# Kernel tuning notes

Measured on AMD Instinct MI355X. Metric: run time of the kernel, lower is better.

Reference implementation:

```python
import jax, jax.numpy as jnp
import numpy as np

D_MODEL = 1024
N_HEADS = 16
D_K = D_MODEL // N_HEADS
MIN_F = 3
MAX_F = 10


def setup_inputs() -> dict:
    key = jax.random.key(0)
    ks = jax.random.split(key, 9)
    B, L = 4, 8192
    x = jax.random.normal(ks[0], (B, L, D_MODEL), jnp.float32)
    def w(k):
        return jax.random.normal(k, (D_MODEL, D_MODEL), jnp.float32) * 0.02
    def b(k):
        return jax.random.normal(k, (D_MODEL,), jnp.float32) * 0.02
    return {
        'x': x,
        'wq': w(ks[1]), 'bq': b(ks[2]),
        'wk': w(ks[3]), 'bk': b(ks[4]),
        'wv': w(ks[5]), 'bv': b(ks[6]),
        'wo': w(ks[7]), 'bo': b(ks[8]),
    }


def _sparsity_score(Q):
    # Q: (B, H, L, d_k)
    l2 = jnp.linalg.norm(Q, axis=-1)
    logp = jax.nn.log_softmax(Q, axis=-1)
    prob = jnp.exp(logp)
    entropy = -jnp.sum(prob * jnp.log(prob + 1e-9), axis=-1)
    var = jnp.var(Q, axis=-1, ddof=1)  # torch.var is unbiased by default
    return 0.5 * l2 + 0.3 * entropy + 0.2 * var


def reference(x, wq, bq, wk, bk, wv, bv, wo, bo):
    B, L, D = x.shape
    H, dk = N_HEADS, D_K
    # torch Linear: y = x @ W.T + b
    Q = (x @ wq.T + bq).reshape(B, L, H, dk).transpose(0, 2, 1, 3)  # (B,H,L,dk)
    K = (x @ wk.T + bk).reshape(B, L, H, dk).transpose(0, 2, 1, 3)
    V = (x @ wv.T + bv).reshape(B, L, H, dk).transpose(0, 2, 1, 3)

    q_scores = _sparsity_score(Q)  # (B,H,L)
    q_std = jnp.std(q_scores, axis=2, keepdims=True, ddof=1)
    q_mean = jnp.mean(q_scores, axis=2, keepdims=True)
    factor = jnp.clip(
        jnp.round(q_std / (q_mean + 1e-6) * MAX_F).astype(jnp.int32),
        MIN_F, MAX_F)  # (B,H,1)
    u = factor[:, 0, 0]  # per-batch k, taken from head 0 (matches torch code)

    # Fixed-size top-k of MAX_F; rows beyond u are masked to zero.
    _, top_idx = jax.lax.top_k(q_scores, MAX_F)  # (B,H,MAX_F)
    mask = (jnp.arange(MAX_F)[None, None, :] < u[:, None, None])  # (B,1->H,MAX_F)

    Q_sparse = jnp.take_along_axis(Q, top_idx[..., None], axis=2)  # (B,H,MAX_F,dk)
    scores = jnp.einsum('bhud,bhld->bhul', Q_sparse, K) / np.sqrt(dk).astype(np.float32)
    attn = jax.nn.softmax(scores, axis=-1)
    out = jnp.einsum('bhul,bhld->bhud', attn, V)  # (B,H,MAX_F,dk)
    out = out * mask[..., None].astype(out.dtype)

    # Scatter back into zeros; top-k indices are distinct per (b,h), so writing
    # masked zeros at the extra indices leaves those rows zero as in torch.
    bi = jnp.arange(B)[:, None, None]
    hi = jnp.arange(H)[None, :, None]
    full = jnp.zeros((B, H, L, dk), out.dtype).at[bi, hi, top_idx].set(out)

    merged = full.transpose(0, 2, 1, 3).reshape(B, L, D)
    return merged @ wo.T + bo
```

## Files before the change

### kernel.cpp

```cpp
#include <hip/hip_runtime.h>
#include <cmath>


typedef short     s16x8 __attribute__((ext_vector_type(8)));
typedef unsigned short u16x8 __attribute__((ext_vector_type(8)));
typedef unsigned short u16x4 __attribute__((ext_vector_type(4)));
typedef float     f32x4 __attribute__((ext_vector_type(4)));

__device__ __forceinline__ unsigned short f2bf(float f) {
    unsigned u = __float_as_uint(f);
    u += 0x7fffu + ((u >> 16) & 1u);
    return (unsigned short)(u >> 16);
}
__device__ __forceinline__ float bf2f(unsigned short s) {
    return __uint_as_float(((unsigned)s) << 16);
}

__device__ __forceinline__ void async16(const void* g, void* l) {
    __builtin_amdgcn_global_load_lds(
        (const __attribute__((address_space(1))) void*)g,
        (__attribute__((address_space(3))) void*)l, 16, 0, 0);
}

__global__ void k_conv(const float* __restrict__ x, const float* __restrict__ wq,
                       const float* __restrict__ wk, const float* __restrict__ wv,
                       unsigned short* __restrict__ xb, unsigned short* __restrict__ wb) {
    size_t i = (size_t)blockIdx.x * 256 + threadIdx.x;
    if (i < 8388608) {
        float4 v = ((const float4*)x)[i];
        ushort4 o; o.x = f2bf(v.x); o.y = f2bf(v.y); o.z = f2bf(v.z); o.w = f2bf(v.w);
        ((ushort4*)xb)[i] = o;
    } else {
        size_t j = i - 8388608;
        size_t wsel = j >> 18, rem = j & 262143;
        const float* src = wsel == 0 ? wq : (wsel == 1 ? wk : wv);
        float4 v = ((const float4*)src)[rem];
        ushort4 o; o.x = f2bf(v.x); o.y = f2bf(v.y); o.z = f2bf(v.z); o.w = f2bf(v.w);
        ((ushort4*)wb)[j] = o;
    }
}

__global__ __launch_bounds__(256) void k_gemm_qkv(
    const unsigned short* __restrict__ xb, const unsigned short* __restrict__ wb,
    const float* __restrict__ bq, const float* __restrict__ bk, const float* __restrict__ bv,
    unsigned short* __restrict__ Kb, unsigned short* __restrict__ Vb,
    float* __restrict__ scores)
{
    __shared__ unsigned short As[128 * 32];
    __shared__ unsigned short Bs[128 * 32];
    int bid = blockIdx.x;
    int mt = bid / 24, rem = bid % 24;
    int wsel = rem >> 3, nt = rem & 7;
    const unsigned short* wbase = wb + ((size_t)wsel << 20) + ((size_t)nt * 128) * 1024;
    const float* bias = wsel == 0 ? bq : (wsel == 1 ? bk : bv);
    unsigned short* outp = wsel == 1 ? Kb : Vb;
    int tid = threadIdx.x, wave = tid >> 6, lane = tid & 63;
    int ml = lane & 15, quad = lane >> 4, wm = wave >> 1, wn = wave & 1;
    int lr = lane >> 2, lc = lane & 3;
    const unsigned short* xbase = xb + ((size_t)mt * 128) * 1024;

    f32x4 acc[4][4] = {};
    for (int k0 = 0; k0 < 1024; k0 += 32) {
#pragma unroll
        for (int s = 0; s < 2; ++s) {
            int seg = wave * 2 + s;
            int row = seg * 16 + lr;
            async16(xbase + (size_t)row * 1024 + k0 + lc * 8, &As[seg * 512]);
            async16(wbase + (size_t)row * 1024 + k0 + lc * 8, &Bs[seg * 512]);
        }
        __builtin_amdgcn_s_waitcnt(0);
        __syncthreads();
        s16x8 a[4], b[4];
#pragma unroll
        for (int i = 0; i < 4; ++i) a[i] = *(const s16x8*)&As[(wm * 64 + i * 16 + ml) * 32 + quad * 8];
#pragma unroll
        for (int j = 0; j < 4; ++j) b[j] = *(const s16x8*)&Bs[(wn * 64 + j * 16 + ml) * 32 + quad * 8];
#pragma unroll
        for (int i = 0; i < 4; ++i)
#pragma unroll
            for (int j = 0; j < 4; ++j)
                acc[i][j] = __builtin_amdgcn_mfma_f32_16x16x32_bf16(a[i], b[j], acc[i][j], 0, 0, 0);
        __syncthreads();
    }

    float bvv[4];
#pragma unroll
    for (int j = 0; j < 4; ++j) bvv[j] = bias[nt * 128 + wn * 64 + j * 16 + ml];

    if (wsel == 0) {
        int hh = nt * 2 + wn;
#pragma unroll
        for (int i = 0; i < 4; ++i) {
#pragma unroll
            for (int r = 0; r < 4; ++r) {
                float q0 = acc[i][0][r] + bvv[0];
                float q1 = acc[i][1][r] + bvv[1];
                float q2 = acc[i][2][r] + bvv[2];
                float q3 = acc[i][3][r] + bvv[3];
                float mx = fmaxf(fmaxf(q0, q1), fmaxf(q2, q3));
                float sm = q0 + q1 + q2 + q3;
                float ss = q0 * q0 + q1 * q1 + q2 * q2 + q3 * q3;
#pragma unroll
                for (int off = 1; off < 16; off <<= 1) {
                    mx = fmaxf(mx, __shfl_xor(mx, off));
                    sm += __shfl_xor(sm, off);
                    ss += __shfl_xor(ss, off);
                }
                float e0 = expf(q0 - mx), e1 = expf(q1 - mx);
                float e2 = expf(q2 - mx), e3 = expf(q3 - mx);
                float S = e0 + e1 + e2 + e3;
#pragma unroll
                for (int off = 1; off < 16; off <<= 1) S += __shfl_xor(S, off);
                float is = 1.f / S;
                float p0 = e0 * is, p1 = e1 * is, p2 = e2 * is, p3 = e3 * is;
                float ent = -p0 * logf(p0 + 1e-9f) - p1 * logf(p1 + 1e-9f)
                            - p2 * logf(p2 + 1e-9f) - p3 * logf(p3 + 1e-9f);
                float mean = sm * (1.f / 64.f);
                float d0 = q0 - mean, d1 = q1 - mean, d2 = q2 - mean, d3 = q3 - mean;
                float var = d0 * d0 + d1 * d1 + d2 * d2 + d3 * d3;
#pragma unroll
                for (int off = 1; off < 16; off <<= 1) {
                    ent += __shfl_xor(ent, off);
                    var += __shfl_xor(var, off);
                }
                if (ml == 0) {
                    float sc = 0.5f * sqrtf(ss) + 0.3f * ent + 0.2f * (var * (1.f / 63.f));
                    int row = mt * 128 + wm * 64 + i * 16 + quad * 4 + r;
                    scores[(size_t)(((row >> 13) << 4) + hh) * 8192 + (row & 8191)] = sc;
                }
            }
        }
    } else {
#pragma unroll
        for (int i = 0; i < 4; ++i) {
            int grow0 = mt * 128 + wm * 64 + i * 16 + quad * 4;
#pragma unroll
            for (int j = 0; j < 4; ++j) {
                int gcol = nt * 128 + wn * 64 + j * 16 + ml;
#pragma unroll
                for (int r = 0; r < 4; ++r)
                    outp[(size_t)(grow0 + r) * 1024 + gcol] = f2bf(acc[i][j][r] + bvv[j]);
            }
        }
    }
}

__global__ __launch_bounds__(1024) void k_cand(const float* __restrict__ scores,
                                               int* __restrict__ cand, int* __restrict__ u)
{
    int pair = blockIdx.x; int t = threadIdx.x;
    __shared__ float  s_lds[8192];
    __shared__ double dred[1024];
    __shared__ float  wvv[16];
    __shared__ int    wii[16];
    const float* sp = scores + (size_t)pair * 8192;
    for (int i = t; i < 8192; i += 1024) s_lds[i] = sp[i];
    __syncthreads();

    if ((pair & 15) == 0) {
        double a0 = 0;
#pragma unroll
        for (int k = 0; k < 8; ++k) a0 += (double)s_lds[t + k * 1024];
        dred[t] = a0; __syncthreads();
        for (int st = 512; st > 0; st >>= 1) { if (t < st) dred[t] += dred[t + st]; __syncthreads(); }
        double mean = dred[0] / 8192.0;
        __syncthreads();
        double a1 = 0;
#pragma unroll
        for (int k = 0; k < 8; ++k) { double d = (double)s_lds[t + k * 1024] - mean; a1 += d * d; }
        dred[t] = a1; __syncthreads();
        for (int st = 512; st > 0; st >>= 1) { if (t < st) dred[t] += dred[t + st]; __syncthreads(); }
        if (t == 0) {
            double sd = sqrt(dred[0] / 8191.0);
            double ratio = sd / (mean + 1e-6) * 10.0;
            int f = (int)rint(ratio);
            f = f < 3 ? 3 : (f > 10 ? 10 : f);
            u[pair >> 4] = f;
        }
        __syncthreads();
    }

    for (int it = 0; it < 16; ++it) {
        float bv = -1e30f; int bi = 0x7fffffff;
#pragma unroll
        for (int k = 0; k < 8; ++k) {
            int i = t + k * 1024;
            float v = s_lds[i];
            if (v > bv || (v == bv && i < bi)) { bv = v; bi = i; }
        }
#pragma unroll
        for (int off = 32; off > 0; off >>= 1) {
            float ov = __shfl_down(bv, off);
            int   oi = __shfl_down(bi, off);
            if (ov > bv || (ov == bv && oi < bi)) { bv = ov; bi = oi; }
        }
        if ((t & 63) == 0) { wvv[t >> 6] = bv; wii[t >> 6] = bi; }
        __syncthreads();
        if (t == 0) {
            float fv = wvv[0]; int fi = wii[0];
            for (int k = 1; k < 16; ++k)
                if (wvv[k] > fv || (wvv[k] == fv && wii[k] < fi)) { fv = wvv[k]; fi = wii[k]; }
            cand[pair * 16 + it] = fi;
            s_lds[fi] = -1e30f;
        }
        __syncthreads();
    }
}

__global__ __launch_bounds__(256) void k_rescore(
    const int* __restrict__ cand, const float* __restrict__ x,
    const float* __restrict__ wq, const float* __restrict__ bq,
    double* __restrict__ cscore, float* __restrict__ cq)
{
    int bid = blockIdx.x;
    int pair = bid >> 4;
    int b = pair >> 4, h = pair & 15;
    int t = threadIdx.x;
    __shared__ float  xrow[1024];
    __shared__ double dred[256];
    __shared__ double qrow[64];

    int l = cand[bid];
    const float* xr = x + ((size_t)b * 8192 + l) * 1024;
    for (int i = t; i < 1024; i += 256) xrow[i] = xr[i];
    __syncthreads();

    int d = t >> 2, ks = t & 3;
    const float* wr = wq + (size_t)(h * 64 + d) * 1024 + ks * 256;
    const float* xs = xrow + ks * 256;
    double p = 0;
    for (int k = 0; k < 256; k += 4) {
        float4 w4 = *(const float4*)(wr + k);
        float4 x4 = *(const float4*)(xs + k);
        p += (double)w4.x * x4.x + (double)w4.y * x4.y +
             (double)w4.z * x4.z + (double)w4.w * x4.w;
    }
    dred[t] = p; __syncthreads();
    if ((t & 3) == 0)
        qrow[t >> 2] = dred[t] + dred[t + 1] + dred[t + 2] + dred[t + 3] + (double)bq[h * 64 + (t >> 2)];
    __syncthreads();

    if (t < 64) {
        double q = qrow[t];
        cq[(size_t)bid * 64 + t] = (float)q;
        double m = q;
#pragma unroll
        for (int off = 32; off > 0; off >>= 1) m = fmax(m, __shfl_down(m, off));
        m = __shfl(m, 0);
        double e = exp(q - m);
        double sum = q, sumsq = q * q, S = e;
#pragma unroll
        for (int off = 32; off > 0; off >>= 1) {
            sum += __shfl_down(sum, off);
            sumsq += __shfl_down(sumsq, off);
            S += __shfl_down(S, off);
        }
        sum = __shfl(sum, 0); sumsq = __shfl(sumsq, 0); S = __shfl(S, 0);
        double pp = e / S;
        double entc = -pp * log(pp + 1e-9);
        double mean = sum / 64.0;
        double dv = q - mean;
        double varc = dv * dv;
#pragma unroll
        for (int off = 32; off > 0; off >>= 1) {
            entc += __shfl_down(entc, off);
            varc += __shfl_down(varc, off);
        }
        if (t == 0)
            cscore[bid] = 0.5 * sqrt(sumsq) + 0.3 * entc + 0.2 * (varc / 63.0);
    }
}

__global__ void k_select(const int* __restrict__ cand, const double* __restrict__ cscore,
                         const float* __restrict__ cq,
                         int* __restrict__ sel, float* __restrict__ selq)
{
    int pair = blockIdx.x; int t = threadIdx.x;
    __shared__ int order[10];
    if (t == 0) {
        bool used[16] = {};
        for (int r = 0; r < 10; ++r) {
            int best = -1;
            for (int c = 0; c < 16; ++c) {
                if (used[c]) continue;
                int ic = pair * 16 + c;
                if (best < 0 || cscore[ic] > cscore[pair * 16 + best] ||
                    (cscore[ic] == cscore[pair * 16 + best] && cand[ic] < cand[pair * 16 + best]))
                    best = c;
            }
            used[best] = true; order[r] = best;
            sel[pair * 10 + r] = cand[pair * 16 + best];
        }
    }
    __syncthreads();
    for (int r = 0; r < 10; ++r)
        selq[((size_t)pair * 10 + r) * 64 + t] = cq[((size_t)pair * 16 + order[r]) * 64 + t];
}

__global__ __launch_bounds__(256) void k_attn_part(
    const unsigned short* __restrict__ Kb, const unsigned short* __restrict__ Vb,
    const float* __restrict__ selq, const int* __restrict__ u,
    float* __restrict__ part)
{
    int bid = blockIdx.x;
    int pair = bid >> 5, chunk = bid & 31;
    int b = pair >> 4, h = pair & 15;
    int uu = u[b];
    int t = threadIdx.x, wave = t >> 6, lane = t & 63;

    __shared__ float q_sh[10][64];
    __shared__ float w_sh[10][256];
    __shared__ unsigned short V_sh[256][68];
    __shared__ float mc_sh[10][2], Sc_sh[10][2];

    size_t kvbase = ((size_t)b * 8192 + (size_t)chunk * 256) * 1024 + h * 64;

    for (int i = t; i < uu * 64; i += 256)
        q_sh[i >> 6][i & 63] = selq[(size_t)pair * 640 + i] * 0.125f;

    const u16x8* kr = (const u16x8*)(Kb + kvbase + (size_t)t * 1024);
    const u16x8* vr = (const u16x8*)(Vb + kvbase + (size_t)t * 1024);
    u16x8 vreg[8];
#pragma unroll
    for (int k8 = 0; k8 < 8; ++k8) vreg[k8] = vr[k8];
#pragma unroll
    for (int k8 = 0; k8 < 8; ++k8) {
        *(u16x4*)&V_sh[t][k8 * 8]     = { vreg[k8][0], vreg[k8][1], vreg[k8][2], vreg[k8][3] };
        *(u16x4*)&V_sh[t][k8 * 8 + 4] = { vreg[k8][4], vreg[k8][5], vreg[k8][6], vreg[k8][7] };
    }
    float krow[64];
#pragma unroll
    for (int k8 = 0; k8 < 8; ++k8) {
        u16x8 kv = kr[k8];
#pragma unroll
        for (int e = 0; e < 8; ++e) krow[k8 * 8 + e] = bf2f(kv[e]);
    }
    __syncthreads();

    for (int rr = 0; rr < uu; ++rr) {
        const float4* qp = (const float4*)q_sh[rr];
        float acc = 0.f;
#pragma unroll
        for (int i4 = 0; i4 < 16; ++i4) {
            float4 q4 = qp[i4];
            acc += q4.x * krow[i4 * 4] + q4.y * krow[i4 * 4 + 1] +
                   q4.z * krow[i4 * 4 + 2] + q4.w * krow[i4 * 4 + 3];
        }
        w_sh[rr][t] = acc;
    }
    __syncthreads();

    for (int rr = wave; rr < uu; rr += 4) {
        float4 wv = *(const float4*)&w_sh[rr][lane * 4];
        float m4 = fmaxf(fmaxf(wv.x, wv.y), fmaxf(wv.z, wv.w));
#pragma unroll
        for (int off = 16; off > 0; off >>= 1) m4 = fmaxf(m4, __shfl_xor(m4, off));
        float e0 = expf(wv.x - m4), e1 = expf(wv.y - m4);
        float e2 = expf(wv.z - m4), e3 = expf(wv.w - m4);
        float s = e0 + e1 + e2 + e3;
#pragma unroll
        for (int off = 16; off > 0; off >>= 1) s += __shfl_xor(s, off);
        float4 ev = { e0, e1, e2, e3 };
        *(float4*)&w_sh[rr][lane * 4] = ev;
        if ((lane & 31) == 0) { int jh = lane >> 5; mc_sh[rr][jh] = m4; Sc_sh[rr][jh] = s; }
    }
    __syncthreads();

    int jh = t >> 7, tt = t & 127, dp = tt & 31;
    for (int rr = tt >> 5; rr < uu; rr += 4) {
        float o0 = 0.f, o1 = 0.f;
        int j0 = jh * 128;
        for (int j = j0; j < j0 + 128; j += 4) {
            float4 w4 = *(const float4*)&w_sh[rr][j];
#pragma unroll
            for (int jj = 0; jj < 4; ++jj) {
                unsigned v = *(const unsigned*)&V_sh[j + jj][dp * 2];
                float w1 = jj == 0 ? w4.x : (jj == 1 ? w4.y : (jj == 2 ? w4.z : w4.w));
                o0 += w1 * __uint_as_float(v << 16);
                o1 += w1 * __uint_as_float(v & 0xffff0000u);
            }
        }
        float* pp = part + (((size_t)pair * 10 + rr) * 64 + chunk * 2 + jh) * 66;
        float2 o2 = { o0, o1 };
        *(float2*)&pp[2 + dp * 2] = o2;
        if (dp == 0) { pp[0] = mc_sh[rr][jh]; pp[1] = Sc_sh[rr][jh]; }
    }
}

__global__ void k_bias(const float* __restrict__ bo, float* __restrict__ out) {
    size_t i = (size_t)blockIdx.x * 256 + threadIdx.x;
    int col4 = (int)(i & 255);
    ((float4*)out)[i] = ((const float4*)bo)[col4];
}

__global__ __launch_bounds__(256) void k_mergescatter(
    const float* __restrict__ part, const int* __restrict__ sel,
    const int* __restrict__ u, const float* __restrict__ wo,
    float* __restrict__ out)
{
    int idx = blockIdx.x; int pair = idx / 10; int r = idx % 10;
    int b = pair >> 4, h = pair & 15;
    if (r >= u[b]) return;
    int t = threadIdx.x;
    __shared__ float a_sh[64];
    if (t < 64) {
        const float* base = part + ((size_t)pair * 10 + r) * 64 * 66;
        float m = -1e30f;
        for (int c = 0; c < 64; ++c) m = fmaxf(m, base[c * 66]);
        float S = 0, o = 0;
        for (int c = 0; c < 64; ++c) {
            float f = expf(base[c * 66] - m);
            S += f * base[c * 66 + 1];
            o += f * base[c * 66 + 2 + t];
        }
        a_sh[t] = o / S;
    }
    __syncthreads();
    int l = sel[pair * 10 + r];
    float* orow = out + ((size_t)b * 8192 + l) * 1024;
    for (int j = t; j < 1024; j += 256) {
        const float* wr = wo + (size_t)j * 1024 + h * 64;
        float acc = 0;
#pragma unroll
        for (int d = 0; d < 64; d += 4) {
            float4 w4 = *(const float4*)(wr + d);
            acc += a_sh[d] * w4.x + a_sh[d + 1] * w4.y + a_sh[d + 2] * w4.z + a_sh[d + 3] * w4.w;
        }
        atomicAdd(orow + j, acc);
    }
}

static constexpr size_t OFF_XB    = 0;
static constexpr size_t OFF_WB    = OFF_XB + 67108864;
static constexpr size_t OFF_KB    = OFF_WB + 6291456;
static constexpr size_t OFF_VB    = OFF_KB + 67108864;
static constexpr size_t OFF_SC    = OFF_VB + 67108864;
static constexpr size_t OFF_U     = OFF_SC + 2097152;
static constexpr size_t OFF_SEL   = OFF_U + 256;
static constexpr size_t OFF_SELQ  = OFF_SEL + 4096;
static constexpr size_t OFF_PART  = OFF_SELQ + 163840;
static constexpr size_t OFF_CAND  = OFF_PART + 10813440;
static constexpr size_t OFF_CSC   = OFF_CAND + 4096;
static constexpr size_t OFF_CQ    = OFF_CSC + 8192;
static constexpr size_t WS_NEED   = OFF_CQ + 262144;

extern "C" void kernel_launch(void* const* d_in, const int* in_sizes, int n_in,
                              void* d_out, int out_size, void* d_ws, size_t ws_size,
                              hipStream_t stream)
{
    const float* x  = (const float*)d_in[0];
    const float* wq = (const float*)d_in[1];
    const float* bq = (const float*)d_in[2];
    const float* wk = (const float*)d_in[3];
    const float* bk = (const float*)d_in[4];
    const float* wv = (const float*)d_in[5];
    const float* bv = (const float*)d_in[6];
    const float* wo = (const float*)d_in[7];
    const float* bo = (const float*)d_in[8];
    float* out = (float*)d_out;

    if (ws_size < WS_NEED) return;

    char* ws = (char*)d_ws;
    unsigned short* xb = (unsigned short*)(ws + OFF_XB);
    unsigned short* wb = (unsigned short*)(ws + OFF_WB);
    unsigned short* Kb = (unsigned short*)(ws + OFF_KB);
    unsigned short* Vb = (unsigned short*)(ws + OFF_VB);
    float*  scores = (float*)(ws + OFF_SC);
    int*    u      = (int*)(ws + OFF_U);
    int*    sel    = (int*)(ws + OFF_SEL);
    float*  selq   = (float*)(ws + OFF_SELQ);
    float*  part   = (float*)(ws + OFF_PART);
    int*    cand   = (int*)(ws + OFF_CAND);
    double* cscore = (double*)(ws + OFF_CSC);
    float*  cq     = (float*)(ws + OFF_CQ);

    k_conv        <<<35840, 256,  0, stream>>>(x, wq, wk, wv, xb, wb);
    k_gemm_qkv    <<<6144,  256,  0, stream>>>(xb, wb, bq, bk, bv, Kb, Vb, scores);
    k_cand        <<<64,    1024, 0, stream>>>(scores, cand, u);
    k_rescore     <<<1024,  256,  0, stream>>>(cand, x, wq, bq, cscore, cq);
    k_select      <<<64,    64,   0, stream>>>(cand, cscore, cq, sel, selq);
    k_attn_part   <<<2048,  256,  0, stream>>>(Kb, Vb, selq, u, part);
    k_bias        <<<32768, 256,  0, stream>>>(bo, out);
    k_mergescatter<<<640,   256,  0, stream>>>(part, sel, u, wo, out);
}
```

Measured before the change: 733.8 us.

## Fuse candidate selection, rescoring and bias init kernels; simplify entropy math

```diff
diff --git a/kernel.cpp b/kernel.cpp
--- a/kernel.cpp
+++ b/kernel.cpp
@@ -22,21 +22,26 @@
         (__attribute__((address_space(3))) void*)l, 16, 0, 0);
 }
 
-__global__ void k_conv(const float* __restrict__ x, const float* __restrict__ wq,
-                       const float* __restrict__ wk, const float* __restrict__ wv,
-                       unsigned short* __restrict__ xb, unsigned short* __restrict__ wb) {
+__global__ void k_convbias(const float* __restrict__ x, const float* __restrict__ wq,
+                           const float* __restrict__ wk, const float* __restrict__ wv,
+                           const float* __restrict__ bo,
+                           unsigned short* __restrict__ xb, unsigned short* __restrict__ wb,
+                           float* __restrict__ out) {
     size_t i = (size_t)blockIdx.x * 256 + threadIdx.x;
     if (i < 8388608) {
         float4 v = ((const float4*)x)[i];
         ushort4 o; o.x = f2bf(v.x); o.y = f2bf(v.y); o.z = f2bf(v.z); o.w = f2bf(v.w);
         ((ushort4*)xb)[i] = o;
-    } else {
+    } else if (i < 9175040) {
         size_t j = i - 8388608;
         size_t wsel = j >> 18, rem = j & 262143;
         const float* src = wsel == 0 ? wq : (wsel == 1 ? wk : wv);
         float4 v = ((const float4*)src)[rem];
         ushort4 o; o.x = f2bf(v.x); o.y = f2bf(v.y); o.z = f2bf(v.z); o.w = f2bf(v.w);
         ((ushort4*)wb)[j] = o;
+    } else {
+        size_t j = i - 9175040;
+        ((float4*)out)[j] = ((const float4*)bo)[j & 255];
     }
 }
 
@@ -106,23 +111,21 @@
                     sm += __shfl_xor(sm, off);
                     ss += __shfl_xor(ss, off);
                 }
-                float e0 = expf(q0 - mx), e1 = expf(q1 - mx);
-                float e2 = expf(q2 - mx), e3 = expf(q3 - mx);
-                float S = e0 + e1 + e2 + e3;
-#pragma unroll
-                for (int off = 1; off < 16; off <<= 1) S += __shfl_xor(S, off);
-                float is = 1.f / S;
-                float p0 = e0 * is, p1 = e1 * is, p2 = e2 * is, p3 = e3 * is;
-                float ent = -p0 * logf(p0 + 1e-9f) - p1 * logf(p1 + 1e-9f)
-                            - p2 * logf(p2 + 1e-9f) - p3 * logf(p3 + 1e-9f);
+                float e0 = __expf(q0 - mx), e1 = __expf(q1 - mx);
+                float e2 = __expf(q2 - mx), e3 = __expf(q3 - mx);
+                float S  = e0 + e1 + e2 + e3;
+                float wsum = e0 * (q0 - mx) + e1 * (q1 - mx) + e2 * (q2 - mx) + e3 * (q3 - mx);
+#pragma unroll
+                for (int off = 1; off < 16; off <<= 1) {
+                    S    += __shfl_xor(S, off);
+                    wsum += __shfl_xor(wsum, off);
+                }
+                float ent = __logf(S) - wsum / S;
                 float mean = sm * (1.f / 64.f);
                 float d0 = q0 - mean, d1 = q1 - mean, d2 = q2 - mean, d3 = q3 - mean;
                 float var = d0 * d0 + d1 * d1 + d2 * d2 + d3 * d3;
 #pragma unroll
-                for (int off = 1; off < 16; off <<= 1) {
-                    ent += __shfl_xor(ent, off);
-                    var += __shfl_xor(var, off);
-                }
+                for (int off = 1; off < 16; off <<= 1) var += __shfl_xor(var, off);
                 if (ml == 0) {
                     float sc = 0.5f * sqrtf(ss) + 0.3f * ent + 0.2f * (var * (1.f / 63.f));
                     int row = mt * 128 + wm * 64 + i * 16 + quad * 4 + r;
@@ -145,14 +148,22 @@
     }
 }
 
-__global__ __launch_bounds__(1024) void k_cand(const float* __restrict__ scores,
-                                               int* __restrict__ cand, int* __restrict__ u)
+__global__ __launch_bounds__(1024) void k_candsel(
+    const float* __restrict__ scores, const float* __restrict__ x,
+    const float* __restrict__ wq, const float* __restrict__ bq,
+    int* __restrict__ u, int* __restrict__ sel, float* __restrict__ selq)
 {
-    int pair = blockIdx.x; int t = threadIdx.x;
+    int pair = blockIdx.x; int b = pair >> 4, h = pair & 15;
+    int t = threadIdx.x;
     __shared__ float  s_lds[8192];
     __shared__ double dred[1024];
     __shared__ float  wvv[16];
     __shared__ int    wii[16];
+    __shared__ int    cand_s[16];
+    __shared__ double dq[16][64];
+    __shared__ double csc[16];
+    __shared__ int    order[10];
+
     const float* sp = scores + (size_t)pair * 8192;
     for (int i = t; i < 8192; i += 1024) s_lds[i] = sp[i];
     __syncthreads();
@@ -200,101 +211,67 @@
             float fv = wvv[0]; int fi = wii[0];
             for (int k = 1; k < 16; ++k)
                 if (wvv[k] > fv || (wvv[k] == fv && wii[k] < fi)) { fv = wvv[k]; fi = wii[k]; }
-            cand[pair * 16 + it] = fi;
+            cand_s[it] = fi;
             s_lds[fi] = -1e30f;
         }
         __syncthreads();
     }
-}
-
-__global__ __launch_bounds__(256) void k_rescore(
-    const int* __restrict__ cand, const float* __restrict__ x,
-    const float* __restrict__ wq, const float* __restrict__ bq,
-    double* __restrict__ cscore, float* __restrict__ cq)
-{
-    int bid = blockIdx.x;
-    int pair = bid >> 4;
-    int b = pair >> 4, h = pair & 15;
-    int t = threadIdx.x;
-    __shared__ float  xrow[1024];
-    __shared__ double dred[256];
-    __shared__ double qrow[64];
-
-    int l = cand[bid];
+
+    int c = t >> 6, d = t & 63;
+    int l = cand_s[c];
     const float* xr = x + ((size_t)b * 8192 + l) * 1024;
-    for (int i = t; i < 1024; i += 256) xrow[i] = xr[i];
-    __syncthreads();
-
-    int d = t >> 2, ks = t & 3;
-    const float* wr = wq + (size_t)(h * 64 + d) * 1024 + ks * 256;
-    const float* xs = xrow + ks * 256;
-    double p = 0;
-    for (int k = 0; k < 256; k += 4) {
+    const float* wr = wq + (size_t)(h * 64 + d) * 1024;
+    double p0 = 0, p1 = 0, p2 = 0, p3 = 0;
+    for (int k = 0; k < 1024; k += 4) {
         float4 w4 = *(const float4*)(wr + k);
-        float4 x4 = *(const float4*)(xs + k);
-        p += (double)w4.x * x4.x + (double)w4.y * x4.y +
-             (double)w4.z * x4.z + (double)w4.w * x4.w;
-    }
-    dred[t] = p; __syncthreads();
-    if ((t & 3) == 0)
-        qrow[t >> 2] = dred[t] + dred[t + 1] + dred[t + 2] + dred[t + 3] + (double)bq[h * 64 + (t >> 2)];
-    __syncthreads();
-
-    if (t < 64) {
-        double q = qrow[t];
-        cq[(size_t)bid * 64 + t] = (float)q;
-        double m = q;
-#pragma unroll
-        for (int off = 32; off > 0; off >>= 1) m = fmax(m, __shfl_down(m, off));
-        m = __shfl(m, 0);
-        double e = exp(q - m);
-        double sum = q, sumsq = q * q, S = e;
-#pragma unroll
-        for (int off = 32; off > 0; off >>= 1) {
-            sum += __shfl_down(sum, off);
-            sumsq += __shfl_down(sumsq, off);
-            S += __shfl_down(S, off);
-        }
-        sum = __shfl(sum, 0); sumsq = __shfl(sumsq, 0); S = __shfl(S, 0);
-        double pp = e / S;
-        double entc = -pp * log(pp + 1e-9);
-        double mean = sum / 64.0;
-        double dv = q - mean;
-        double varc = dv * dv;
-#pragma unroll
-        for (int off = 32; off > 0; off >>= 1) {
-            entc += __shfl_down(entc, off);
-            varc += __shfl_down(varc, off);
-        }
-        if (t == 0)
-            cscore[bid] = 0.5 * sqrt(sumsq) + 0.3 * entc + 0.2 * (varc / 63.0);
-    }
-}
-
-__global__ void k_select(const int* __restrict__ cand, const double* __restrict__ cscore,
-                         const float* __restrict__ cq,
-                         int* __restrict__ sel, float* __restrict__ selq)
-{
-    int pair = blockIdx.x; int t = threadIdx.x;
-    __shared__ int order[10];
+        float4 x4 = *(const float4*)(xr + k);
+        p0 += (double)w4.x * x4.x; p1 += (double)w4.y * x4.y;
+        p2 += (double)w4.z * x4.z; p3 += (double)w4.w * x4.w;
+    }
+    double q = p0 + p1 + p2 + p3 + (double)bq[h * 64 + d];
+    dq[c][d] = q;
+    double m = q;
+#pragma unroll
+    for (int off = 32; off > 0; off >>= 1) m = fmax(m, __shfl_down(m, off));
+    m = __shfl(m, 0);
+    double e = exp(q - m);
+    double sum = q, sumsq = q * q, S = e;
+#pragma unroll
+    for (int off = 32; off > 0; off >>= 1) {
+        sum += __shfl_down(sum, off);
+        sumsq += __shfl_down(sumsq, off);
+        S += __shfl_down(S, off);
+    }
+    sum = __shfl(sum, 0); sumsq = __shfl(sumsq, 0); S = __shfl(S, 0);
+    double pp = e / S;
+    double entc = -pp * log(pp + 1e-9);
+    double mean = sum / 64.0;
+    double dv = q - mean;
+    double varc = dv * dv;
+#pragma unroll
+    for (int off = 32; off > 0; off >>= 1) {
+        entc += __shfl_down(entc, off);
+        varc += __shfl_down(varc, off);
+    }
+    if (d == 0) csc[c] = 0.5 * sqrt(sumsq) + 0.3 * entc + 0.2 * (varc / 63.0);
+    __syncthreads();
+
     if (t == 0) {
         bool used[16] = {};
         for (int r = 0; r < 10; ++r) {
             int best = -1;
-            for (int c = 0; c < 16; ++c) {
-                if (used[c]) continue;
-                int ic = pair * 16 + c;
-                if (best < 0 || cscore[ic] > cscore[pair * 16 + best] ||
-                    (cscore[ic] == cscore[pair * 16 + best] && cand[ic] < cand[pair * 16 + best]))
-                    best = c;
+            for (int cc = 0; cc < 16; ++cc) {
+                if (used[cc]) continue;
+                if (best < 0 || csc[cc] > csc[best] ||
+                    (csc[cc] == csc[best] && cand_s[cc] < cand_s[best])) best = cc;
             }
             used[best] = true; order[r] = best;
-            sel[pair * 10 + r] = cand[pair * 16 + best];
-        }
-    }
-    __syncthreads();
-    for (int r = 0; r < 10; ++r)
-        selq[((size_t)pair * 10 + r) * 64 + t] = cq[((size_t)pair * 16 + order[r]) * 64 + t];
+            sel[pair * 10 + r] = cand_s[best];
+        }
+    }
+    __syncthreads();
+    if (t < 640)
+        selq[(size_t)pair * 640 + t] = (float)dq[order[t >> 6]][t & 63];
 }
 
 __global__ __launch_bounds__(256) void k_attn_part(
@@ -355,8 +332,8 @@
         float m4 = fmaxf(fmaxf(wv.x, wv.y), fmaxf(wv.z, wv.w));
 #pragma unroll
         for (int off = 16; off > 0; off >>= 1) m4 = fmaxf(m4, __shfl_xor(m4, off));
-        float e0 = expf(wv.x - m4), e1 = expf(wv.y - m4);
-        float e2 = expf(wv.z - m4), e3 = expf(wv.w - m4);
+        float e0 = __expf(wv.x - m4), e1 = __expf(wv.y - m4);
+        float e2 = __expf(wv.z - m4), e3 = __expf(wv.w - m4);
         float s = e0 + e1 + e2 + e3;
 #pragma unroll
         for (int off = 16; off > 0; off >>= 1) s += __shfl_xor(s, off);
@@ -385,12 +362,6 @@
         *(float2*)&pp[2 + dp * 2] = o2;
         if (dp == 0) { pp[0] = mc_sh[rr][jh]; pp[1] = Sc_sh[rr][jh]; }
     }
-}
-
-__global__ void k_bias(const float* __restrict__ bo, float* __restrict__ out) {
-    size_t i = (size_t)blockIdx.x * 256 + threadIdx.x;
-    int col4 = (int)(i & 255);
-    ((float4*)out)[i] = ((const float4*)bo)[col4];
 }
 
 __global__ __launch_bounds__(256) void k_mergescatter(
@@ -409,7 +380,7 @@
         for (int c = 0; c < 64; ++c) m = fmaxf(m, base[c * 66]);
         float S = 0, o = 0;
         for (int c = 0; c < 64; ++c) {
-            float f = expf(base[c * 66] - m);
+            float f = __expf(base[c * 66] - m);
             S += f * base[c * 66 + 1];
             o += f * base[c * 66 + 2 + t];
         }
@@ -439,10 +410,7 @@
 static constexpr size_t OFF_SEL   = OFF_U + 256;
 static constexpr size_t OFF_SELQ  = OFF_SEL + 4096;
 static constexpr size_t OFF_PART  = OFF_SELQ + 163840;
-static constexpr size_t OFF_CAND  = OFF_PART + 10813440;
-static constexpr size_t OFF_CSC   = OFF_CAND + 4096;
-static constexpr size_t OFF_CQ    = OFF_CSC + 8192;
-static constexpr size_t WS_NEED   = OFF_CQ + 262144;
+static constexpr size_t WS_NEED   = OFF_PART + 10813440;
 
 extern "C" void kernel_launch(void* const* d_in, const int* in_sizes, int n_in,
                               void* d_out, int out_size, void* d_ws, size_t ws_size,
@@ -471,16 +439,10 @@
     int*    sel    = (int*)(ws + OFF_SEL);
     float*  selq   = (float*)(ws + OFF_SELQ);
     float*  part   = (float*)(ws + OFF_PART);
-    int*    cand   = (int*)(ws + OFF_CAND);
-    double* cscore = (double*)(ws + OFF_CSC);
-    float*  cq     = (float*)(ws + OFF_CQ);
-
-    k_conv        <<<35840, 256,  0, stream>>>(x, wq, wk, wv, xb, wb);
+
+    k_convbias    <<<68608, 256,  0, stream>>>(x, wq, wk, wv, bo, xb, wb, out);
     k_gemm_qkv    <<<6144,  256,  0, stream>>>(xb, wb, bq, bk, bv, Kb, Vb, scores);
-    k_cand        <<<64,    1024, 0, stream>>>(scores, cand, u);
-    k_rescore     <<<1024,  256,  0, stream>>>(cand, x, wq, bq, cscore, cq);
-    k_select      <<<64,    64,   0, stream>>>(cand, cscore, cq, sel, selq);
+    k_candsel     <<<64,    1024, 0, stream>>>(scores, x, wq, bq, u, sel, selq);
     k_attn_part   <<<2048,  256,  0, stream>>>(Kb, Vb, selq, u, part);
-    k_bias        <<<32768, 256,  0, stream>>>(bo, out);
     k_mergescatter<<<640,   256,  0, stream>>>(part, sel, u, wo, out);
 }
```

After: 839.0 us. 14.3% more time.

## Split sparsity scoring out of QKV GEMM and fuse bias fill into conversion

Applied to the files above, without the earlier changes.

```diff
diff --git a/kernel.cpp b/kernel.cpp
--- a/kernel.cpp
+++ b/kernel.cpp
@@ -22,29 +22,33 @@
         (__attribute__((address_space(3))) void*)l, 16, 0, 0);
 }
 
-__global__ void k_conv(const float* __restrict__ x, const float* __restrict__ wq,
-                       const float* __restrict__ wk, const float* __restrict__ wv,
-                       unsigned short* __restrict__ xb, unsigned short* __restrict__ wb) {
+__global__ void k_convbias(const float* __restrict__ x, const float* __restrict__ wq,
+                           const float* __restrict__ wk, const float* __restrict__ wv,
+                           const float* __restrict__ bo,
+                           unsigned short* __restrict__ xb, unsigned short* __restrict__ wb,
+                           float* __restrict__ out) {
     size_t i = (size_t)blockIdx.x * 256 + threadIdx.x;
     if (i < 8388608) {
         float4 v = ((const float4*)x)[i];
         ushort4 o; o.x = f2bf(v.x); o.y = f2bf(v.y); o.z = f2bf(v.z); o.w = f2bf(v.w);
         ((ushort4*)xb)[i] = o;
-    } else {
+    } else if (i < 9175040) {
         size_t j = i - 8388608;
         size_t wsel = j >> 18, rem = j & 262143;
         const float* src = wsel == 0 ? wq : (wsel == 1 ? wk : wv);
         float4 v = ((const float4*)src)[rem];
         ushort4 o; o.x = f2bf(v.x); o.y = f2bf(v.y); o.z = f2bf(v.z); o.w = f2bf(v.w);
         ((ushort4*)wb)[j] = o;
+    } else {
+        size_t j = i - 9175040;
+        ((float4*)out)[j] = ((const float4*)bo)[j & 255];
     }
 }
 
 __global__ __launch_bounds__(256) void k_gemm_qkv(
     const unsigned short* __restrict__ xb, const unsigned short* __restrict__ wb,
     const float* __restrict__ bq, const float* __restrict__ bk, const float* __restrict__ bv,
-    unsigned short* __restrict__ Kb, unsigned short* __restrict__ Vb,
-    float* __restrict__ scores)
+    unsigned short* __restrict__ Qb, unsigned short* __restrict__ Kb, unsigned short* __restrict__ Vb)
 {
     __shared__ unsigned short As[128 * 32];
     __shared__ unsigned short Bs[128 * 32];
@@ -53,7 +57,7 @@
     int wsel = rem >> 3, nt = rem & 7;
     const unsigned short* wbase = wb + ((size_t)wsel << 20) + ((size_t)nt * 128) * 1024;
     const float* bias = wsel == 0 ? bq : (wsel == 1 ? bk : bv);
-    unsigned short* outp = wsel == 1 ? Kb : Vb;
+    unsigned short* outp = wsel == 0 ? Qb : (wsel == 1 ? Kb : Vb);
     int tid = threadIdx.x, wave = tid >> 6, lane = tid & 63;
     int ml = lane & 15, quad = lane >> 4, wm = wave >> 1, wn = wave & 1;
     int lr = lane >> 2, lc = lane & 3;
@@ -82,66 +86,61 @@
                 acc[i][j] = __builtin_amdgcn_mfma_f32_16x16x32_bf16(a[i], b[j], acc[i][j], 0, 0, 0);
         __syncthreads();
     }
-
-    float bvv[4];
-#pragma unroll
-    for (int j = 0; j < 4; ++j) bvv[j] = bias[nt * 128 + wn * 64 + j * 16 + ml];
-
-    if (wsel == 0) {
-        int hh = nt * 2 + wn;
-#pragma unroll
-        for (int i = 0; i < 4; ++i) {
-#pragma unroll
-            for (int r = 0; r < 4; ++r) {
-                float q0 = acc[i][0][r] + bvv[0];
-                float q1 = acc[i][1][r] + bvv[1];
-                float q2 = acc[i][2][r] + bvv[2];
-                float q3 = acc[i][3][r] + bvv[3];
-                float mx = fmaxf(fmaxf(q0, q1), fmaxf(q2, q3));
-                float sm = q0 + q1 + q2 + q3;
-                float ss = q0 * q0 + q1 * q1 + q2 * q2 + q3 * q3;
-#pragma unroll
-                for (int off = 1; off < 16; off <<= 1) {
-                    mx = fmaxf(mx, __shfl_xor(mx, off));
-                    sm += __shfl_xor(sm, off);
-                    ss += __shfl_xor(ss, off);
-                }
-                float e0 = expf(q0 - mx), e1 = expf(q1 - mx);
-                float e2 = expf(q2 - mx), e3 = expf(q3 - mx);
-                float S = e0 + e1 + e2 + e3;
-#pragma unroll
-                for (int off = 1; off < 16; off <<= 1) S += __shfl_xor(S, off);
-                float is = 1.f / S;
-                float p0 = e0 * is, p1 = e1 * is, p2 = e2 * is, p3 = e3 * is;
-                float ent = -p0 * logf(p0 + 1e-9f) - p1 * logf(p1 + 1e-9f)
-                            - p2 * logf(p2 + 1e-9f) - p3 * logf(p3 + 1e-9f);
-                float mean = sm * (1.f / 64.f);
-                float d0 = q0 - mean, d1 = q1 - mean, d2 = q2 - mean, d3 = q3 - mean;
-                float var = d0 * d0 + d1 * d1 + d2 * d2 + d3 * d3;
-#pragma unroll
-                for (int off = 1; off < 16; off <<= 1) {
-                    ent += __shfl_xor(ent, off);
-                    var += __shfl_xor(var, off);
-                }
-                if (ml == 0) {
-                    float sc = 0.5f * sqrtf(ss) + 0.3f * ent + 0.2f * (var * (1.f / 63.f));
-                    int row = mt * 128 + wm * 64 + i * 16 + quad * 4 + r;
-                    scores[(size_t)(((row >> 13) << 4) + hh) * 8192 + (row & 8191)] = sc;
-                }
-            }
-        }
-    } else {
-#pragma unroll
-        for (int i = 0; i < 4; ++i) {
-            int grow0 = mt * 128 + wm * 64 + i * 16 + quad * 4;
-#pragma unroll
-            for (int j = 0; j < 4; ++j) {
-                int gcol = nt * 128 + wn * 64 + j * 16 + ml;
-#pragma unroll
-                for (int r = 0; r < 4; ++r)
-                    outp[(size_t)(grow0 + r) * 1024 + gcol] = f2bf(acc[i][j][r] + bvv[j]);
-            }
-        }
+#pragma unroll
+    for (int i = 0; i < 4; ++i) {
+        int grow0 = mt * 128 + wm * 64 + i * 16 + quad * 4;
+#pragma unroll
+        for (int j = 0; j < 4; ++j) {
+            int gcol = nt * 128 + wn * 64 + j * 16 + ml;
+            float bvv = bias[gcol];
+#pragma unroll
+            for (int r = 0; r < 4; ++r)
+                outp[(size_t)(grow0 + r) * 1024 + gcol] = f2bf(acc[i][j][r] + bvv);
+        }
+    }
+}
+
+__global__ void k_score(const unsigned short* __restrict__ Qb, float* __restrict__ scores) {
+    int gid = blockIdx.x * 256 + threadIdx.x;
+    int item = gid >> 3, sub = gid & 7;
+    int r = item >> 4, h = item & 15;
+    u16x8 v = ((const u16x8*)(Qb + (size_t)r * 1024 + h * 64))[sub];
+    float q[8];
+#pragma unroll
+    for (int e = 0; e < 8; ++e) q[e] = bf2f(v[e]);
+
+    float mx = q[0];
+#pragma unroll
+    for (int e = 1; e < 8; ++e) mx = fmaxf(mx, q[e]);
+#pragma unroll
+    for (int off = 1; off < 8; off <<= 1) mx = fmaxf(mx, __shfl_xor(mx, off));
+
+    float sm = 0.f, ss = 0.f, S = 0.f, wsum = 0.f;
+#pragma unroll
+    for (int e = 0; e < 8; ++e) {
+        float qe = q[e];
+        sm += qe; ss += qe * qe;
+        float ex = __expf(qe - mx);
+        S += ex; wsum += ex * (qe - mx);
+    }
+#pragma unroll
+    for (int off = 1; off < 8; off <<= 1) {
+        sm += __shfl_xor(sm, off);
+        ss += __shfl_xor(ss, off);
+        S  += __shfl_xor(S, off);
+        wsum += __shfl_xor(wsum, off);
+    }
+    float mean = sm * (1.f / 64.f);
+    float vs = 0.f;
+#pragma unroll
+    for (int e = 0; e < 8; ++e) { float d = q[e] - mean; vs += d * d; }
+#pragma unroll
+    for (int off = 1; off < 8; off <<= 1) vs += __shfl_xor(vs, off);
+
+    if (sub == 0) {
+        float ent = __logf(S) - wsum / S;
+        float sc = 0.5f * sqrtf(ss) + 0.3f * ent + 0.2f * (vs * (1.f / 63.f));
+        scores[(size_t)(((r >> 13) << 4) + h) * 8192 + (r & 8191)] = sc;
     }
 }
 
@@ -355,8 +354,8 @@
         float m4 = fmaxf(fmaxf(wv.x, wv.y), fmaxf(wv.z, wv.w));
 #pragma unroll
         for (int off = 16; off > 0; off >>= 1) m4 = fmaxf(m4, __shfl_xor(m4, off));
-        float e0 = expf(wv.x - m4), e1 = expf(wv.y - m4);
-        float e2 = expf(wv.z - m4), e3 = expf(wv.w - m4);
+        float e0 = __expf(wv.x - m4), e1 = __expf(wv.y - m4);
+        float e2 = __expf(wv.z - m4), e3 = __expf(wv.w - m4);
         float s = e0 + e1 + e2 + e3;
 #pragma unroll
         for (int off = 16; off > 0; off >>= 1) s += __shfl_xor(s, off);
@@ -385,12 +384,6 @@
         *(float2*)&pp[2 + dp * 2] = o2;
         if (dp == 0) { pp[0] = mc_sh[rr][jh]; pp[1] = Sc_sh[rr][jh]; }
     }
-}
-
-__global__ void k_bias(const float* __restrict__ bo, float* __restrict__ out) {
-    size_t i = (size_t)blockIdx.x * 256 + threadIdx.x;
-    int col4 = (int)(i & 255);
-    ((float4*)out)[i] = ((const float4*)bo)[col4];
 }
 
 __global__ __launch_bounds__(256) void k_mergescatter(
@@ -409,7 +402,7 @@
         for (int c = 0; c < 64; ++c) m = fmaxf(m, base[c * 66]);
         float S = 0, o = 0;
         for (int c = 0; c < 64; ++c) {
-            float f = expf(base[c * 66] - m);
+            float f = __expf(base[c * 66] - m);
             S += f * base[c * 66 + 1];
             o += f * base[c * 66 + 2 + t];
         }
@@ -432,7 +425,8 @@
 
 static constexpr size_t OFF_XB    = 0;
 static constexpr size_t OFF_WB    = OFF_XB + 67108864;
-static constexpr size_t OFF_KB    = OFF_WB + 6291456;
+static constexpr size_t OFF_QB    = OFF_WB + 6291456;
+static constexpr size_t OFF_KB    = OFF_QB + 67108864;
 static constexpr size_t OFF_VB    = OFF_KB + 67108864;
 static constexpr size_t OFF_SC    = OFF_VB + 67108864;
 static constexpr size_t OFF_U     = OFF_SC + 2097152;
@@ -464,6 +458,7 @@
     char* ws = (char*)d_ws;
     unsigned short* xb = (unsigned short*)(ws + OFF_XB);
     unsigned short* wb = (unsigned short*)(ws + OFF_WB);
+    unsigned short* Qb = (unsigned short*)(ws + OFF_QB);
     unsigned short* Kb = (unsigned short*)(ws + OFF_KB);
     unsigned short* Vb = (unsigned short*)(ws + OFF_VB);
     float*  scores = (float*)(ws + OFF_SC);
@@ -475,12 +470,12 @@
     double* cscore = (double*)(ws + OFF_CSC);
     float*  cq     = (float*)(ws + OFF_CQ);
 
-    k_conv        <<<35840, 256,  0, stream>>>(x, wq, wk, wv, xb, wb);
-    k_gemm_qkv    <<<6144,  256,  0, stream>>>(xb, wb, bq, bk, bv, Kb, Vb, scores);
+    k_convbias    <<<68608, 256,  0, stream>>>(x, wq, wk, wv, bo, xb, wb, out);
+    k_gemm_qkv    <<<6144,  256,  0, stream>>>(xb, wb, bq, bk, bv, Qb, Kb, Vb);
+    k_score       <<<16384, 256,  0, stream>>>(Qb, scores);
     k_cand        <<<64,    1024, 0, stream>>>(scores, cand, u);
     k_rescore     <<<1024,  256,  0, stream>>>(cand, x, wq, bq, cscore, cq);
     k_select      <<<64,    64,   0, stream>>>(cand, cscore, cq, sel, selq);
     k_attn_part   <<<2048,  256,  0, stream>>>(Kb, Vb, selq, u, part);
-    k_bias        <<<32768, 256,  0, stream>>>(bo, out);
     k_mergescatter<<<640,   256,  0, stream>>>(part, sel, u, wo, out);
 }
```

Result: no change. 737.6 us (+0.5%).
